# Kernel tuning notes

Hardware: AMD Instinct MI355X
Metric: run time of the kernel (lower is better)

The kernel has to match this reference:

```python
import jax, jax.numpy as jnp
import numpy as np

B, T, E, D = 4, 4096, 1024, 64

def setup_inputs() -> dict:
    key = jax.random.key(0)
    kx, kq, kk, kv = jax.random.split(key, 4)
    # kaiming_normal_ on [E, D] (fan_in = E in torch default mode='fan_in'):
    std = (2.0 / E) ** 0.5
    return {
        "x": jax.random.normal(kx, (B, T, E), dtype=jnp.float32),
        "Wq": jax.random.normal(kq, (E, D), dtype=jnp.float32) * std,
        "Wk": jax.random.normal(kk, (E, D), dtype=jnp.float32) * std,
        "Wv": jax.random.normal(kv, (E, D), dtype=jnp.float32) * std,
    }

def reference(x, Wq, Wk, Wv):
    q = jnp.einsum('bte,ei->bti', x, Wq)
    k = jnp.einsum('bte,ei->bti', x, Wk)
    v = jnp.einsum('bte,ei->bti', x, Wv)
    scale = 1.0 / jnp.sqrt(jnp.asarray(q.shape[-1], q.dtype))
    qk = jnp.einsum('bti,bTi->btT', q, k)  # [B, T, T] full score matrix
    s = jax.nn.softmax(qk * scale, axis=-1)
    return jnp.einsum('btT,bTi->bti', s, v)
```

## Files before the change

### kernel.cpp

```cpp
#include <hip/hip_runtime.h>
#include <stdint.h>


#define T_DIM 4096
#define E_DIM 1024
#define D_DIM 64
#define NROWS 16384

typedef __bf16 bf16x8 __attribute__((ext_vector_type(8)));
typedef __bf16 bf16x4 __attribute__((ext_vector_type(4)));
typedef float  f32x4  __attribute__((ext_vector_type(4)));

__global__ void conv_w(const float* __restrict__ Wq, const float* __restrict__ Wk,
                       const float* __restrict__ Wv, __bf16* __restrict__ wF)
{
    int idx = blockIdx.x * 256 + threadIdx.x;
    if (idx >= 196608) return;
    int j    = idx & 7;
    int lane = (idx >> 3) & 63;
    int n    = (idx >> 9) & 3;
    int ktG  = (idx >> 11) & 31;
    int m    = idx >> 16;
    int d = n * 16 + (lane & 15);
    int e = ktG * 32 + (lane >> 4) * 8 + j;
    const float* W = (m == 0) ? Wq : (m == 1) ? Wk : Wv;
    float v = W[e * D_DIM + d];
    if (m == 0) v *= 0.125f;
    wF[idx] = (__bf16)v;
}

__global__ __launch_bounds__(256) void aaaa_qkvpj(const float* __restrict__ x,
        const __bf16* __restrict__ wF, __bf16* __restrict__ QKVf)
{
    __shared__ __bf16 xs[64][72];

    const int tid  = threadIdx.x;
    const int lane = tid & 63;
    const int w    = tid >> 6;
    const int lrow = lane & 15;
    const int lq   = lane >> 4;
    const int bI   = blockIdx.x;
    const int r0   = bI * 64;
    const float* xbase = x + (long)r0 * E_DIM;
    const __bf16* wl   = wF + lane * 8;

    f32x4 acc[3][4] = {};

    f32x4 r0v, r1v, r2v, r3v;
    {
        int f0 = tid, f1 = 256 + tid, f2 = 512 + tid, f3 = 768 + tid;
        r0v = *(const f32x4*)(xbase + (f0 >> 4) * E_DIM + (f0 & 15) * 4);
        r1v = *(const f32x4*)(xbase + (f1 >> 4) * E_DIM + (f1 & 15) * 4);
        r2v = *(const f32x4*)(xbase + (f2 >> 4) * E_DIM + (f2 & 15) * 4);
        r3v = *(const f32x4*)(xbase + (f3 >> 4) * E_DIM + (f3 & 15) * 4);
    }

    #pragma unroll 1
    for (int ks = 0; ks < 16; ++ks) {
        __syncthreads();
        {
            int f0 = tid, f1 = 256 + tid, f2 = 512 + tid, f3 = 768 + tid;
            bf16x4 b0, b1, b2, b3;
            b0[0]=(__bf16)r0v[0]; b0[1]=(__bf16)r0v[1]; b0[2]=(__bf16)r0v[2]; b0[3]=(__bf16)r0v[3];
            b1[0]=(__bf16)r1v[0]; b1[1]=(__bf16)r1v[1]; b1[2]=(__bf16)r1v[2]; b1[3]=(__bf16)r1v[3];
            b2[0]=(__bf16)r2v[0]; b2[1]=(__bf16)r2v[1]; b2[2]=(__bf16)r2v[2]; b2[3]=(__bf16)r2v[3];
            b3[0]=(__bf16)r3v[0]; b3[1]=(__bf16)r3v[1]; b3[2]=(__bf16)r3v[2]; b3[3]=(__bf16)r3v[3];
            *(bf16x4*)&xs[f0 >> 4][(f0 & 15) * 4] = b0;
            *(bf16x4*)&xs[f1 >> 4][(f1 & 15) * 4] = b1;
            *(bf16x4*)&xs[f2 >> 4][(f2 & 15) * 4] = b2;
            *(bf16x4*)&xs[f3 >> 4][(f3 & 15) * 4] = b3;
        }
        if (ks < 15) {
            const float* nb = xbase + (ks + 1) * 64;
            int f0 = tid, f1 = 256 + tid, f2 = 512 + tid, f3 = 768 + tid;
            r0v = *(const f32x4*)(nb + (f0 >> 4) * E_DIM + (f0 & 15) * 4);
            r1v = *(const f32x4*)(nb + (f1 >> 4) * E_DIM + (f1 & 15) * 4);
            r2v = *(const f32x4*)(nb + (f2 >> 4) * E_DIM + (f2 & 15) * 4);
            r3v = *(const f32x4*)(nb + (f3 >> 4) * E_DIM + (f3 & 15) * 4);
        }
        __syncthreads();
        #pragma unroll
        for (int kh = 0; kh < 2; ++kh) {
            bf16x8 a = *(const bf16x8*)&xs[w * 16 + lrow][kh * 32 + lq * 8];
            #pragma unroll
            for (int m = 0; m < 3; ++m)
                #pragma unroll
                for (int n = 0; n < 4; ++n) {
                    bf16x8 b = *(const bf16x8*)(wl + (((m * 32 + ks * 2 + kh) * 4 + n) << 9));
                    acc[m][n] = __builtin_amdgcn_mfma_f32_16x16x32_bf16(a, b, acc[m][n], 0, 0, 0);
                }
        }
    }

    #pragma unroll
    for (int m = 0; m < 3; ++m) {
        __syncthreads();
        #pragma unroll
        for (int n = 0; n < 4; ++n)
            #pragma unroll
            for (int j = 0; j < 4; ++j)
                xs[w * 16 + lq * 4 + j][n * 16 + lrow] = (__bf16)acc[m][n][j];
        __syncthreads();
        if (m == 0) {
            #pragma unroll
            for (int fi = 0; fi < 2; ++fi) {
                bf16x8 v = *(const bf16x8*)&xs[w * 16 + lrow][fi * 32 + lq * 8];
                *(bf16x8*)&QKVf[(long)((bI * 4 + w) * 2 + fi) * 512 + lane * 8] = v;
            }
        } else if (m == 1) {
            #pragma unroll
            for (int fi = 0; fi < 2; ++fi) {
                bf16x8 v = *(const bf16x8*)&xs[w * 16 + lrow][fi * 32 + lq * 8];
                *(bf16x8*)&QKVf[(long)(2048 + bI * 8 + fi * 4 + w) * 512 + lane * 8] = v;
            }
        } else {
            #pragma unroll
            for (int fi = 0; fi < 2; ++fi) {
                bf16x8 v;
                #pragma unroll
                for (int j = 0; j < 8; ++j)
                    v[j] = xs[fi * 32 + lq * 8 + j][w * 16 + lrow];
                *(bf16x8*)&QKVf[(long)(4096 + bI * 8 + fi * 4 + w) * 512 + lane * 8] = v;
            }
        }
    }
}

__global__ __launch_bounds__(256) void flash_attn(const __bf16* __restrict__ QKVf,
        float* __restrict__ Op, float* __restrict__ lp,
        float* __restrict__ out, int ntile, int direct)
{
    __shared__ __bf16 pl[4][32][72];

    const int tid  = threadIdx.x;
    const int lane = tid & 63;
    const int w    = tid >> 6;
    const int lrow = lane & 15;
    const int lq   = lane >> 4;
    const int bid  = blockIdx.x;
    const int sp   = bid >> 7;
    const int qb   = bid & 127;
    const int b    = qb >> 5;
    const int qt   = qb & 31;
    const int rg   = b * 256 + qt * 8 + w * 2;
    const int grow0 = b * 4096 + qt * 128 + w * 32;

    bf16x8 qf[2][2];
    #pragma unroll
    for (int mi = 0; mi < 2; ++mi)
        #pragma unroll
        for (int kh = 0; kh < 2; ++kh)
            qf[mi][kh] = *(const bf16x8*)&QKVf[(long)((rg + mi) * 2 + kh) * 512 + lane * 8];

    f32x4 oacc[2][4] = {};
    float lsum[2][4] = {};

    const __bf16* kbase = QKVf + (long)(2048 + b * 64 * 8) * 512 + lane * 8;
    const __bf16* vbase = QKVf + (long)(4096 + b * 64 * 8) * 512 + lane * 8;

    const int kv0 = sp * ntile;
    #pragma unroll 1
    for (int kv = kv0; kv < kv0 + ntile; ++kv) {
        const __bf16* kf = kbase + ((long)kv << 12);
        const __bf16* vf = vbase + ((long)kv << 12);

        bf16x8 kfr[2][4];
        #pragma unroll
        for (int kh = 0; kh < 2; ++kh)
            #pragma unroll
            for (int n = 0; n < 4; ++n)
                kfr[kh][n] = *(const bf16x8*)(kf + ((kh * 4 + n) << 9));

        f32x4 sacc[2][4] = {};
        #pragma unroll
        for (int mi = 0; mi < 2; ++mi)
            #pragma unroll
            for (int n = 0; n < 4; ++n)
                #pragma unroll
                for (int kh = 0; kh < 2; ++kh)
                    sacc[mi][n] = __builtin_amdgcn_mfma_f32_16x16x32_bf16(
                        qf[mi][kh], kfr[kh][n], sacc[mi][n], 0, 0, 0);

        bf16x8 vfr[2][4];
        #pragma unroll
        for (int kh = 0; kh < 2; ++kh)
            #pragma unroll
            for (int n = 0; n < 4; ++n)
                vfr[kh][n] = *(const bf16x8*)(vf + ((kh * 4 + n) << 9));

        #pragma unroll
        for (int mi = 0; mi < 2; ++mi)
            #pragma unroll
            for (int n = 0; n < 4; ++n)
                #pragma unroll
                for (int j = 0; j < 4; ++j) {
                    float pv = __expf(sacc[mi][n][j]);
                    lsum[mi][j] += pv;
                    pl[w][mi * 16 + lq * 4 + j][n * 16 + lrow] = (__bf16)pv;
                }

        #pragma unroll
        for (int mi = 0; mi < 2; ++mi)
            #pragma unroll
            for (int kh = 0; kh < 2; ++kh) {
                bf16x8 pa = *(const bf16x8*)&pl[w][mi * 16 + lrow][kh * 32 + lq * 8];
                #pragma unroll
                for (int n = 0; n < 4; ++n)
                    oacc[mi][n] = __builtin_amdgcn_mfma_f32_16x16x32_bf16(
                        pa, vfr[kh][n], oacc[mi][n], 0, 0, 0);
            }
    }

    #pragma unroll
    for (int msk = 1; msk < 16; msk <<= 1)
        #pragma unroll
        for (int mi = 0; mi < 2; ++mi)
            #pragma unroll
            for (int j = 0; j < 4; ++j)
                lsum[mi][j] += __shfl_xor(lsum[mi][j], msk);

    if (direct) {
        #pragma unroll
        for (int mi = 0; mi < 2; ++mi)
            #pragma unroll
            for (int j = 0; j < 4; ++j) {
                float inv = 1.0f / lsum[mi][j];
                long row = grow0 + mi * 16 + lq * 4 + j;
                #pragma unroll
                for (int n = 0; n < 4; ++n)
                    out[row * 64 + n * 16 + lrow] = oacc[mi][n][j] * inv;
            }
    } else {
        #pragma unroll
        for (int mi = 0; mi < 2; ++mi)
            #pragma unroll
            for (int j = 0; j < 4; ++j) {
                long prow = (long)sp * NROWS + grow0 + mi * 16 + lq * 4 + j;
                #pragma unroll
                for (int n = 0; n < 4; ++n)
                    Op[prow * 64 + n * 16 + lrow] = oacc[mi][n][j];
                if (lrow == 0) lp[prow] = lsum[mi][j];
            }
    }
}

template <int NS>
__device__ __forceinline__ void combine_body(const float* Op, const float* lp,
        float* out, int idx)
{
    int d    = idx & 63;
    int grow = idx >> 6;
    float L = 0.f, O = 0.f;
    #pragma unroll
    for (int s = 0; s < NS; ++s) {
        L += lp[s * NROWS + grow];
        O += Op[((long)s * NROWS + grow) * 64 + d];
    }
    out[idx] = O / L;
}

__global__ __launch_bounds__(256) void ab_combine(const float* __restrict__ Op,
        const float* __restrict__ lp, float* __restrict__ out, int nsplit)
{
    int idx = blockIdx.x * 256 + threadIdx.x;
    if (nsplit == 8) combine_body<8>(Op, lp, out, idx);
    else             combine_body<4>(Op, lp, out, idx);
}

extern "C" void kernel_launch(void* const* d_in, const int* in_sizes, int n_in,
                              void* d_out, int out_size, void* d_ws, size_t ws_size,
                              hipStream_t stream)
{
    const float* x  = (const float*)d_in[0];
    const float* Wq = (const float*)d_in[1];
    const float* Wk = (const float*)d_in[2];
    const float* Wv = (const float*)d_in[3];
    float* out = (float*)d_out;

    char* wsb = (char*)d_ws;
    __bf16* wF   = (__bf16*)wsb;
    __bf16* QKVf = (__bf16*)(wsb + 524288);
    float*  lp   = (float*)(wsb + 6815744);
    float*  Op   = (float*)(wsb + 7340032);
    const size_t NEED8 = 7340032ull + 33554432ull;
    const size_t NEED4 = 7340032ull + 16777216ull;

    conv_w    <<<768, 256, 0, stream>>>(Wq, Wk, Wv, wF);
    aaaa_qkvpj<<<256, 256, 0, stream>>>(x, wF, QKVf);
    if (ws_size >= NEED8) {
        flash_attn<<<1024, 256, 0, stream>>>(QKVf, Op, lp, nullptr, 8, 0);
        ab_combine<<<4096, 256, 0, stream>>>(Op, lp, out, 8);
    } else if (ws_size >= NEED4) {
        flash_attn<<<512, 256, 0, stream>>>(QKVf, Op, lp, nullptr, 16, 0);
        ab_combine<<<4096, 256, 0, stream>>>(Op, lp, out, 4);
    } else {
        flash_attn<<<128, 256, 0, stream>>>(QKVf, nullptr, nullptr, out, 64, 1);
    }
}
```

Before: 164.6 us.

## Split QKV projection into 16-row blocks with per-wave output fragments and double-buffered LDS

```diff
diff --git a/kernel.cpp b/kernel.cpp
--- a/kernel.cpp
+++ b/kernel.cpp
@@ -29,10 +29,12 @@
     wF[idx] = (__bf16)v;
 }
 
+#define XPAD 80
 __global__ __launch_bounds__(256) void aaaa_qkvpj(const float* __restrict__ x,
         const __bf16* __restrict__ wF, __bf16* __restrict__ QKVf)
 {
-    __shared__ __bf16 xs[64][72];
+    __shared__ __bf16 xs[2][16][XPAD];
+    __shared__ __bf16 cb[3][16][XPAD];
 
     const int tid  = threadIdx.x;
     const int lane = tid & 63;
@@ -40,87 +42,88 @@
     const int lrow = lane & 15;
     const int lq   = lane >> 4;
     const int bI   = blockIdx.x;
-    const int r0   = bI * 64;
-    const float* xbase = x + (long)r0 * E_DIM;
-    const __bf16* wl   = wF + lane * 8;
-
-    f32x4 acc[3][4] = {};
-
-    f32x4 r0v, r1v, r2v, r3v;
+    const float* xbase = x + (long)(bI * 16) * E_DIM;
+
+    int fid0 = w * 3;
+    const __bf16* wp[3];
+    int fm[3], fn[3];
+    #pragma unroll
+    for (int i = 0; i < 3; ++i) {
+        int fid = fid0 + i;
+        fm[i] = fid >> 2; fn[i] = fid & 3;
+        wp[i] = wF + ((long)(fm[i] * 32 * 4 + fn[i]) << 9) + lane * 8;
+    }
+
+    const int srow = tid >> 4;
+    const int scol = (tid & 15) * 4;
+
+    f32x4 acc[3] = {};
+    f32x4 pre;
+
+    pre = *(const f32x4*)(xbase + srow * E_DIM + scol);
     {
-        int f0 = tid, f1 = 256 + tid, f2 = 512 + tid, f3 = 768 + tid;
-        r0v = *(const f32x4*)(xbase + (f0 >> 4) * E_DIM + (f0 & 15) * 4);
-        r1v = *(const f32x4*)(xbase + (f1 >> 4) * E_DIM + (f1 & 15) * 4);
-        r2v = *(const f32x4*)(xbase + (f2 >> 4) * E_DIM + (f2 & 15) * 4);
-        r3v = *(const f32x4*)(xbase + (f3 >> 4) * E_DIM + (f3 & 15) * 4);
-    }
+        bf16x4 bv;
+        bv[0] = (__bf16)pre[0]; bv[1] = (__bf16)pre[1];
+        bv[2] = (__bf16)pre[2]; bv[3] = (__bf16)pre[3];
+        *(bf16x4*)&xs[0][srow][scol] = bv;
+    }
+    pre = *(const f32x4*)(xbase + srow * E_DIM + 64 + scol);
+    __syncthreads();
 
     #pragma unroll 1
     for (int ks = 0; ks < 16; ++ks) {
-        __syncthreads();
-        {
-            int f0 = tid, f1 = 256 + tid, f2 = 512 + tid, f3 = 768 + tid;
-            bf16x4 b0, b1, b2, b3;
-            b0[0]=(__bf16)r0v[0]; b0[1]=(__bf16)r0v[1]; b0[2]=(__bf16)r0v[2]; b0[3]=(__bf16)r0v[3];
-            b1[0]=(__bf16)r1v[0]; b1[1]=(__bf16)r1v[1]; b1[2]=(__bf16)r1v[2]; b1[3]=(__bf16)r1v[3];
-            b2[0]=(__bf16)r2v[0]; b2[1]=(__bf16)r2v[1]; b2[2]=(__bf16)r2v[2]; b2[3]=(__bf16)r2v[3];
-            b3[0]=(__bf16)r3v[0]; b3[1]=(__bf16)r3v[1]; b3[2]=(__bf16)r3v[2]; b3[3]=(__bf16)r3v[3];
-            *(bf16x4*)&xs[f0 >> 4][(f0 & 15) * 4] = b0;
-            *(bf16x4*)&xs[f1 >> 4][(f1 & 15) * 4] = b1;
-            *(bf16x4*)&xs[f2 >> 4][(f2 & 15) * 4] = b2;
-            *(bf16x4*)&xs[f3 >> 4][(f3 & 15) * 4] = b3;
+        const int cur = ks & 1;
+        #pragma unroll
+        for (int kh = 0; kh < 2; ++kh) {
+            bf16x8 a = *(const bf16x8*)&xs[cur][lrow][kh * 32 + lq * 8];
+            int koff = (ks * 2 + kh) * 2048;
+            #pragma unroll
+            for (int i = 0; i < 3; ++i) {
+                bf16x8 b = *(const bf16x8*)(wp[i] + koff);
+                acc[i] = __builtin_amdgcn_mfma_f32_16x16x32_bf16(a, b, acc[i], 0, 0, 0);
+            }
         }
         if (ks < 15) {
-            const float* nb = xbase + (ks + 1) * 64;
-            int f0 = tid, f1 = 256 + tid, f2 = 512 + tid, f3 = 768 + tid;
-            r0v = *(const f32x4*)(nb + (f0 >> 4) * E_DIM + (f0 & 15) * 4);
-            r1v = *(const f32x4*)(nb + (f1 >> 4) * E_DIM + (f1 & 15) * 4);
-            r2v = *(const f32x4*)(nb + (f2 >> 4) * E_DIM + (f2 & 15) * 4);
-            r3v = *(const f32x4*)(nb + (f3 >> 4) * E_DIM + (f3 & 15) * 4);
+            bf16x4 bv;
+            bv[0] = (__bf16)pre[0]; bv[1] = (__bf16)pre[1];
+            bv[2] = (__bf16)pre[2]; bv[3] = (__bf16)pre[3];
+            *(bf16x4*)&xs[cur ^ 1][srow][scol] = bv;
+            if (ks < 14)
+                pre = *(const f32x4*)(xbase + srow * E_DIM + (ks + 2) * 64 + scol);
         }
         __syncthreads();
-        #pragma unroll
-        for (int kh = 0; kh < 2; ++kh) {
-            bf16x8 a = *(const bf16x8*)&xs[w * 16 + lrow][kh * 32 + lq * 8];
-            #pragma unroll
-            for (int m = 0; m < 3; ++m)
-                #pragma unroll
-                for (int n = 0; n < 4; ++n) {
-                    bf16x8 b = *(const bf16x8*)(wl + (((m * 32 + ks * 2 + kh) * 4 + n) << 9));
-                    acc[m][n] = __builtin_amdgcn_mfma_f32_16x16x32_bf16(a, b, acc[m][n], 0, 0, 0);
-                }
-        }
-    }
-
-    #pragma unroll
-    for (int m = 0; m < 3; ++m) {
-        __syncthreads();
-        #pragma unroll
-        for (int n = 0; n < 4; ++n)
-            #pragma unroll
-            for (int j = 0; j < 4; ++j)
-                xs[w * 16 + lq * 4 + j][n * 16 + lrow] = (__bf16)acc[m][n][j];
-        __syncthreads();
-        if (m == 0) {
-            #pragma unroll
-            for (int fi = 0; fi < 2; ++fi) {
-                bf16x8 v = *(const bf16x8*)&xs[w * 16 + lrow][fi * 32 + lq * 8];
-                *(bf16x8*)&QKVf[(long)((bI * 4 + w) * 2 + fi) * 512 + lane * 8] = v;
-            }
-        } else if (m == 1) {
-            #pragma unroll
-            for (int fi = 0; fi < 2; ++fi) {
-                bf16x8 v = *(const bf16x8*)&xs[w * 16 + lrow][fi * 32 + lq * 8];
-                *(bf16x8*)&QKVf[(long)(2048 + bI * 8 + fi * 4 + w) * 512 + lane * 8] = v;
-            }
-        } else {
-            #pragma unroll
-            for (int fi = 0; fi < 2; ++fi) {
+    }
+
+    #pragma unroll
+    for (int i = 0; i < 3; ++i)
+        #pragma unroll
+        for (int j = 0; j < 4; ++j)
+            cb[fm[i]][lq * 4 + j][fn[i] * 16 + lrow] = (__bf16)acc[i][j];
+    __syncthreads();
+
+    const int tile = bI >> 2;
+    const int q    = bI & 3;
+
+    #pragma unroll
+    for (int fi = 0; fi < 2; ++fi) {
+        bf16x8 v = *(const bf16x8*)&cb[0][lrow][fi * 32 + lq * 8];
+        *(bf16x8*)&QKVf[(long)(bI * 2 + fi) * 512 + lane * 8] = v;
+    }
+    #pragma unroll
+    for (int fi = 0; fi < 2; ++fi) {
+        bf16x8 v = *(const bf16x8*)&cb[1][lrow][fi * 32 + lq * 8];
+        *(bf16x8*)&QKVf[(long)(2048 + tile * 8 + fi * 4 + q) * 512 + lane * 8] = v;
+    }
+    {
+        const int kh = q >> 1;
+        if ((lq >> 1) == (q & 1)) {
+            #pragma unroll
+            for (int n = 0; n < 4; ++n) {
                 bf16x8 v;
                 #pragma unroll
                 for (int j = 0; j < 8; ++j)
-                    v[j] = xs[fi * 32 + lq * 8 + j][w * 16 + lrow];
-                *(bf16x8*)&QKVf[(long)(4096 + bI * 8 + fi * 4 + w) * 512 + lane * 8] = v;
+                    v[j] = cb[2][(lq & 1) * 8 + j][n * 16 + lrow];
+                *(bf16x8*)&QKVf[(long)(4096 + tile * 8 + kh * 4 + n) * 512 + lane * 8] = v;
             }
         }
     }
@@ -286,7 +289,7 @@
     const size_t NEED4 = 7340032ull + 16777216ull;
 
     conv_w    <<<768, 256, 0, stream>>>(Wq, Wk, Wv, wF);
-    aaaa_qkvpj<<<256, 256, 0, stream>>>(x, wF, QKVf);
+    aaaa_qkvpj<<<1024, 256, 0, stream>>>(x, wF, QKVf);
     if (ws_size >= NEED8) {
         flash_attn<<<1024, 256, 0, stream>>>(QKVf, Op, lp, nullptr, 8, 0);
         ab_combine<<<4096, 256, 0, stream>>>(Op, lp, out, 8);
```

Measured after the change: 158.1 us. -4.0%, faster.
